# Performance work log

Hardware: AMD Instinct MI355X
Metric: run time of the kernel (lower is better)

The kernel has to match this reference:

```python
import jax, jax.numpy as jnp
import numpy as np

NUM_HEADS = 16
EPS = 1e-12  # matches torch F.normalize eps


def _l2_normalize(x):
    n = jnp.sqrt(jnp.sum(x * x, axis=-1, keepdims=True))
    return x / jnp.maximum(n, EPS)


def setup_inputs() -> dict:
    key = jax.random.key(0)
    ks = jax.random.split(key, 9)
    B, L, S, D = 4, 4096, 4096, 1024
    s = 1.0 / np.sqrt(D)
    return {
        "q": jax.random.normal(ks[0], (B, L, D), jnp.float32),
        "k": jax.random.normal(ks[1], (B, S, D), jnp.float32),
        "v": jax.random.normal(ks[2], (B, S, D), jnp.float32),
        "Wq": jax.random.normal(ks[3], (D, D), jnp.float32) * s,
        "bq": jax.random.normal(ks[4], (D,), jnp.float32) * 0.01,
        "Wk": jax.random.normal(ks[5], (D, D), jnp.float32) * s,
        "bk": jax.random.normal(ks[6], (D,), jnp.float32) * 0.01,
        "Wv": jax.random.normal(ks[7], (D, D), jnp.float32) * s,
        "bv": jax.random.normal(ks[8], (D,), jnp.float32) * 0.01,
    }


def reference(q, k, v, Wq, bq, Wk, bk, Wv, bv):
    B = q.shape[0]
    H = NUM_HEADS
    # Linear projections (torch Linear: x @ W^T + b)
    qp = q @ Wq.T + bq  # [B, L, D]
    kp = k @ Wk.T + bk  # [B, S, D]
    vp = v @ Wv.T + bv  # [B, S, D]
    # Split heads: [B, T, H, i] -> [B, H, T, i]
    def split(x):
        Bx, T, D = x.shape
        return x.reshape(Bx, T, H, D // H).transpose(0, 2, 1, 3)
    qh = split(qp)
    kh = _l2_normalize(split(kp))
    vh = _l2_normalize(split(vp))
    # No softmax -> exact reassociation: (q k^T) v == q (k^T v)
    kv = jnp.einsum('bhsi,bhsj->bhij', kh, vh)  # [B, H, i, i]
    xh = jnp.einsum('bhli,bhij->bhlj', qh, kv)  # [B, H, L, i]
    # Merge heads: [B, H, L, i] -> [B, L, H*i]
    Bx, Hh, L, I = xh.shape
    return xh.transpose(0, 2, 1, 3).reshape(Bx, L, Hh * I)
```

## Files before the change

### kernel.cpp

```cpp
#include <hip/hip_runtime.h>
#include <hip/hip_bf16.h>
#include <stdint.h>

typedef __attribute__((ext_vector_type(8))) short bf16x8;
typedef __attribute__((ext_vector_type(4))) float f32x4;
typedef __attribute__((ext_vector_type(8))) unsigned short ushort8;

__device__ __forceinline__ float bf2f(unsigned short u) {
  union { unsigned int i; float f; } x; x.i = ((unsigned int)u) << 16; return x.f;
}
__device__ __forceinline__ unsigned short f2bf(float f) {
  union { __hip_bfloat16 h; unsigned short u; } x; x.h = __float2bfloat16(f); return x.u;
}

__device__ __forceinline__ void gload_lds16(const void* g, void* l) {
  __builtin_amdgcn_global_load_lds((__attribute__((address_space(1))) const void*)g,
                                   (__attribute__((address_space(3))) void*)l, 16, 0, 0);
}

__global__ __launch_bounds__(256) void cvt_kernel(const float* __restrict__ in,
                                                  unsigned short* __restrict__ out,
                                                  int n8) {
  int i = blockIdx.x * 256 + threadIdx.x;
  if (i >= n8) return;
  const float4* p = (const float4*)(in + (size_t)i * 8);
  float4 a = p[0], b = p[1];
  ushort8 o;
  o[0] = f2bf(a.x); o[1] = f2bf(a.y); o[2] = f2bf(a.z); o[3] = f2bf(a.w);
  o[4] = f2bf(b.x); o[5] = f2bf(b.y); o[6] = f2bf(b.z); o[7] = f2bf(b.w);
  *(ushort8*)(out + (size_t)i * 8) = o;
}

__global__ __launch_bounds__(256) void cvt2_kernel(const float* __restrict__ a,
                                                   const float* __restrict__ b,
                                                   unsigned short* __restrict__ oa,
                                                   unsigned short* __restrict__ ob,
                                                   int n8) {
  const float* in = blockIdx.y ? b : a;
  unsigned short* out = blockIdx.y ? ob : oa;
  int i = blockIdx.x * 256 + threadIdx.x;
  if (i >= n8) return;
  const float4* p = (const float4*)(in + (size_t)i * 8);
  float4 x = p[0], y = p[1];
  ushort8 o;
  o[0] = f2bf(x.x); o[1] = f2bf(x.y); o[2] = f2bf(x.z); o[3] = f2bf(x.w);
  o[4] = f2bf(y.x); o[5] = f2bf(y.y); o[6] = f2bf(y.z); o[7] = f2bf(y.w);
  *(ushort8*)(out + (size_t)i * 8) = o;
}

__global__ __launch_bounds__(256) void cvt3w_kernel(const float* __restrict__ a,
                                                    const float* __restrict__ b,
                                                    const float* __restrict__ c,
                                                    unsigned short* __restrict__ oa,
                                                    unsigned short* __restrict__ ob,
                                                    unsigned short* __restrict__ oc,
                                                    int n8) {
  const float* in = blockIdx.y == 0 ? a : blockIdx.y == 1 ? b : c;
  unsigned short* out = blockIdx.y == 0 ? oa : blockIdx.y == 1 ? ob : oc;
  int i = blockIdx.x * 256 + threadIdx.x;
  if (i >= n8) return;
  const float4* p = (const float4*)(in + (size_t)i * 8);
  float4 x = p[0], y = p[1];
  ushort8 o;
  o[0] = f2bf(x.x); o[1] = f2bf(x.y); o[2] = f2bf(x.z); o[3] = f2bf(x.w);
  o[4] = f2bf(y.x); o[5] = f2bf(y.y); o[6] = f2bf(y.z); o[7] = f2bf(y.w);
  *(ushort8*)(out + (size_t)i * 8) = o;
}

__device__ __forceinline__ void gemm256_loop(
    const unsigned short* __restrict__ A,
    const unsigned short* __restrict__ B,
    int bm, int bn,
    unsigned short (*As)[256][32], unsigned short (*Bs)[256][32],
    f32x4 (*acc)[4]) {
  const int tid = threadIdx.x;
  const int widx = tid >> 6, lane = tid & 63;
  const int wr = widx >> 2, wc = widx & 3;
  const int fr = lane & 15, fkg = lane >> 4;
  const int pgo = (fkg ^ ((fr >> 1) & 3)) * 8;
  const int srow = lane >> 2;
  const int sg = ((lane & 3) ^ ((lane >> 3) & 3)) * 8;

  const size_t abase = (size_t)(bm * 256) * 1024;
  const size_t bbase = (size_t)(bn * 256) * 1024;

  bf16x8 aF[8], bF[4];

#define STG_A(bufi, kh, kt)                                                                \
  {                                                                                        \
    gload_lds16(A + abase + (size_t)(widx * 16 + srow) * 1024 + (kt) * 64 + (kh) * 32 + sg,\
                &As[(bufi) * 2 + (kh)][widx * 16][0]);                                     \
    gload_lds16(A + abase + (size_t)(128 + widx * 16 + srow) * 1024 + (kt) * 64 + (kh) * 32 + sg, \
                &As[(bufi) * 2 + (kh)][128 + widx * 16][0]);                               \
  }
#define STG_B(bufi, kh, kt)                                                                \
  {                                                                                        \
    gload_lds16(B + bbase + (size_t)(widx * 16 + srow) * 1024 + (kt) * 64 + (kh) * 32 + sg,\
                &Bs[(bufi) * 2 + (kh)][widx * 16][0]);                                     \
    gload_lds16(B + bbase + (size_t)(128 + widx * 16 + srow) * 1024 + (kt) * 64 + (kh) * 32 + sg, \
                &Bs[(bufi) * 2 + (kh)][128 + widx * 16][0]);                               \
  }
#define LDA(bufi, ks)                                                                      \
  _Pragma("unroll") for (int m = 0; m < 8; ++m)                                            \
      aF[m] = *(const bf16x8*)&As[(bufi) * 2 + (ks)][wr * 128 + m * 16 + fr][pgo];
#define LDBALL(bufi, ks)                                                                   \
  _Pragma("unroll") for (int n = 0; n < 4; ++n)                                            \
      bF[n] = *(const bf16x8*)&Bs[(bufi) * 2 + (ks)][wc * 64 + n * 16 + fr][pgo];
#define MMALL()                                                                            \
  {                                                                                        \
    __builtin_amdgcn_s_setprio(1);                                                         \
    _Pragma("unroll") for (int m = 0; m < 8; ++m)                                          \
        _Pragma("unroll") for (int n = 0; n < 4; ++n)                                      \
            acc[m][n] = __builtin_amdgcn_mfma_f32_16x16x32_bf16(aF[m], bF[n], acc[m][n], 0, 0, 0); \
    __builtin_amdgcn_s_setprio(0);                                                         \
  }
#define BARM() asm volatile("s_barrier" ::: "memory")
#define VMW(N) asm volatile("s_waitcnt vmcnt(" #N ")" ::: "memory")

  STG_A(0, 0, 0); STG_B(0, 0, 0);
  STG_A(0, 1, 0); STG_B(0, 1, 0);
  STG_A(1, 0, 1); STG_B(1, 0, 1);
  VMW(4);
  BARM();

  for (int i = 0; i < 8; ++i) {
    const int t1s = 2 * i + 1, u0 = 2 * i + 2, u1 = 2 * i + 3;
    const bool st = (i < 7);
    LDA(0, 0); LDBALL(0, 0); STG_A(1, 1, t1s); STG_B(1, 1, t1s);
    BARM(); MMALL(); BARM();
    LDA(0, 1); LDBALL(0, 1); if (st) { STG_A(0, 0, u0); STG_B(0, 0, u0); }
    BARM(); MMALL();
    if (st) { VMW(4); } else { VMW(0); }
    BARM();
    LDA(1, 0); LDBALL(1, 0); if (st) { STG_A(0, 1, u0); STG_B(0, 1, u0); }
    BARM(); MMALL(); BARM();
    LDA(1, 1); LDBALL(1, 1); if (st) { STG_A(1, 0, u1); STG_B(1, 0, u1); }
    BARM(); MMALL();
    if (st) { VMW(4); } else { VMW(0); }
    BARM();
  }
#undef STG_A
#undef STG_B
#undef LDA
#undef LDBALL
#undef MMALL
#undef BARM
#undef VMW
}

__global__ __launch_bounds__(512, 1) void proj_norm_kernel(
    const unsigned short* __restrict__ A0, const unsigned short* __restrict__ A1,
    const unsigned short* __restrict__ B0, const unsigned short* __restrict__ B1,
    const float* __restrict__ bias0, const float* __restrict__ bias1,
    unsigned short* __restrict__ C0, unsigned short* __restrict__ C1) {
  __shared__ unsigned short As[4][256][32];
  __shared__ unsigned short Bs[4][256][32];
  const int flat = (blockIdx.z * 64 + blockIdx.y) * 4 + blockIdx.x;
  const int swz = (flat & 7) * 64 + (flat >> 3);
  const int zz = swz >> 8;
  const int rem = swz & 255;
  const int bm = rem >> 2, bn = rem & 3;
  const unsigned short* A = zz ? A1 : A0;
  const unsigned short* B = zz ? B1 : B0;
  const float* bias = zz ? bias1 : bias0;
  unsigned short* C = zz ? C1 : C0;

  f32x4 acc[8][4];
#pragma unroll
  for (int m = 0; m < 8; ++m)
#pragma unroll
    for (int n = 0; n < 4; ++n) acc[m][n] = (f32x4){0.f, 0.f, 0.f, 0.f};

  gemm256_loop(A, B, bm, bn, As, Bs, acc);

  const int tid = threadIdx.x, widx = tid >> 6, lane = tid & 63;
  const int wr = widx >> 2, wc = widx & 3;
  const int fr = lane & 15, g4 = (lane >> 4) * 4;

  float bsv[4];
#pragma unroll
  for (int n = 0; n < 4; ++n) bsv[n] = bias[bn * 256 + wc * 64 + n * 16 + fr];
#pragma unroll
  for (int m = 0; m < 8; ++m) {
    float val[4][4];
    float inv[4];
#pragma unroll
    for (int j = 0; j < 4; ++j) {
      float s = 0.f;
#pragma unroll
      for (int n = 0; n < 4; ++n) {
        val[n][j] = acc[m][n][j] + bsv[n];
        s += val[n][j] * val[n][j];
      }
      s += __shfl_xor(s, 1); s += __shfl_xor(s, 2);
      s += __shfl_xor(s, 4); s += __shfl_xor(s, 8);
      inv[j] = 1.f / fmaxf(sqrtf(s), 1e-12f);
    }
#pragma unroll
    for (int n = 0; n < 4; ++n) {
      const int col = bn * 256 + wc * 64 + n * 16 + fr;
#pragma unroll
      for (int j = 0; j < 4; ++j) {
        const int row = bm * 256 + wr * 128 + m * 16 + g4 + j;
        C[(size_t)row * 1024 + col] = f2bf(val[n][j] * inv[j]);
      }
    }
  }
}

__global__ __launch_bounds__(512, 1) void final_fold_kernel(
    const unsigned short* __restrict__ A,
    const unsigned short* __restrict__ Wqb,
    const float* __restrict__ bq,
    const unsigned short* __restrict__ kvT,
    float* __restrict__ out) {
  __shared__ __align__(16) unsigned char smem[163840];
  unsigned short (*As)[256][32] = (unsigned short (*)[256][32])smem;
  unsigned short (*Bs)[256][32] = (unsigned short (*)[256][32])(smem + 65536);

  const int flat = blockIdx.y * 4 + blockIdx.x;
  const int swz = (flat & 7) * 32 + (flat >> 3);
  const int bm = swz >> 2, bn = swz & 3;
  const int bB = bm >> 4;

  const int tid = threadIdx.x, widx = tid >> 6, lane = tid & 63;
  const int wr = widx >> 2, wc = widx & 3;
  const int fr = lane & 15, fkg = lane >> 4, g4 = fkg * 4;

#pragma unroll
  for (int t = 0; t < 4; ++t) {
    int unit = t * 512 + tid;
    int h = unit >> 9;
    int jr = (unit >> 3) & 63;
    int g = unit & 7;
    ushort8 vvv = *(const ushort8*)(kvT +
        ((size_t)(bB * 16 + bn * 4 + h) * 4096) + jr * 64 + g * 8);
    *(ushort8*)(smem + 131072 + h * 8192 + jr * 128 + ((g ^ (jr & 7)) * 16)) = vvv;
  }
  __syncthreads();

  f32x4 acc[8][4];
#pragma unroll
  for (int m = 0; m < 8; ++m)
#pragma unroll
    for (int n = 0; n < 4; ++n) acc[m][n] = (f32x4){0.f, 0.f, 0.f, 0.f};

  gemm256_loop(A, Wqb, bm, bn, As, Bs, acc);

  {
    float bsv[4];
#pragma unroll
    for (int n = 0; n < 4; ++n) bsv[n] = bq[bn * 256 + wc * 64 + n * 16 + fr];
#pragma unroll
    for (int m = 0; m < 8; ++m)
#pragma unroll
      for (int n = 0; n < 4; ++n)
#pragma unroll
        for (int j = 0; j < 4; ++j) {
          float v = acc[m][n][j] + bsv[n];
          int r = m * 16 + g4 + j;
          int c = n * 16 + fr;
          *(unsigned short*)(smem + widx * 16384 + r * 128 +
                             (((c >> 3) ^ (r & 7)) * 16) + (c & 7) * 2) = f2bf(v);
        }
  }
  __syncthreads();

  f32x4 acc2[8][4];
#pragma unroll
  for (int m = 0; m < 8; ++m)
#pragma unroll
    for (int n = 0; n < 4; ++n) acc2[m][n] = (f32x4){0.f, 0.f, 0.f, 0.f};

#pragma unroll
  for (int ks = 0; ks < 2; ++ks) {
    bf16x8 a2[8], b2[4];
#pragma unroll
    for (int m = 0; m < 8; ++m)
      a2[m] = *(const bf16x8*)(smem + widx * 16384 + (m * 16 + fr) * 128 +
                               (((ks * 4 + fkg) ^ (fr & 7)) * 16));
#pragma unroll
    for (int n = 0; n < 4; ++n)
      b2[n] = *(const bf16x8*)(smem + 131072 + wc * 8192 + (n * 16 + fr) * 128 +
                               (((ks * 4 + fkg) ^ (fr & 7)) * 16));
#pragma unroll
    for (int m = 0; m < 8; ++m)
#pragma unroll
      for (int n = 0; n < 4; ++n)
        acc2[m][n] = __builtin_amdgcn_mfma_f32_16x16x32_bf16(a2[m], b2[n], acc2[m][n], 0, 0, 0);
  }

#pragma unroll
  for (int n = 0; n < 4; ++n) {
    const int col = bn * 256 + wc * 64 + n * 16 + fr;
#pragma unroll
    for (int m = 0; m < 8; ++m)
#pragma unroll
      for (int j = 0; j < 4; ++j) {
        const int row = bm * 256 + wr * 128 + m * 16 + g4 + j;
        out[(size_t)row * 1024 + col] = acc2[m][n][j];
      }
  }
}

__global__ __launch_bounds__(256) void kv_part_kernel(const unsigned short* __restrict__ kh,
                                                      const unsigned short* __restrict__ vh,
                                                      float* __restrict__ kvp) {
  const int chunk = blockIdx.x, h = blockIdx.y, b = blockIdx.z;
  __shared__ unsigned short khT[64][264];
  __shared__ unsigned short vhT[64][264];
  const int tid = threadIdx.x, wid = tid >> 6, lane = tid & 63;
  const int fr = lane & 15, fk = (lane >> 4) * 8, g4 = (lane >> 4) * 4;

  const int jb = tid & 7, sb = tid >> 3;
  const size_t base = ((size_t)b * 4096 + chunk * 256) * 1024 + h * 64;
  {
    ushort8 rk[8], rv[8];
#pragma unroll
    for (int u = 0; u < 8; ++u) {
      rk[u] = *(const ushort8*)(kh + base + (size_t)(sb * 8 + u) * 1024 + jb * 8);
      rv[u] = *(const ushort8*)(vh + base + (size_t)(sb * 8 + u) * 1024 + jb * 8);
    }
#pragma unroll
    for (int jj = 0; jj < 8; ++jj) {
      ushort8 ck, cv;
#pragma unroll
      for (int u = 0; u < 8; ++u) { ck[u] = rk[u][jj]; cv[u] = rv[u][jj]; }
      *(ushort8*)&khT[jb * 8 + jj][sb * 8] = ck;
      *(ushort8*)&vhT[jb * 8 + jj][sb * 8] = cv;
    }
  }
  __syncthreads();

  f32x4 acc2[4];
#pragma unroll
  for (int n = 0; n < 4; ++n) acc2[n] = (f32x4){0.f, 0.f, 0.f, 0.f};
#pragma unroll
  for (int ks = 0; ks < 8; ++ks) {
    bf16x8 a2 = *(const bf16x8*)&khT[wid * 16 + fr][ks * 32 + fk];
    bf16x8 b2[4];
#pragma unroll
    for (int jt = 0; jt < 4; ++jt) b2[jt] = *(const bf16x8*)&vhT[jt * 16 + fr][ks * 32 + fk];
#pragma unroll
    for (int jt = 0; jt < 4; ++jt)
      acc2[jt] = __builtin_amdgcn_mfma_f32_16x16x32_bf16(a2, b2[jt], acc2[jt], 0, 0, 0);
  }
  float* dst = kvp + ((size_t)chunk * 64 + b * 16 + h) * 4096;
#pragma unroll
  for (int jt = 0; jt < 4; ++jt)
#pragma unroll
    for (int jj = 0; jj < 4; ++jj)
      dst[(wid * 16 + g4 + jj) * 64 + jt * 16 + fr] = acc2[jt][jj];
}

__global__ __launch_bounds__(256) void kvt_reduce_kernel(const float* __restrict__ kvp,
                                                         unsigned short* __restrict__ kvT) {
  const int bh = blockIdx.x;
  for (int e = threadIdx.x; e < 4096; e += 256) {
    float s = 0.f;
#pragma unroll
    for (int c = 0; c < 16; ++c) s += kvp[((size_t)c * 64 + bh) * 4096 + e];
    int i = e >> 6, j = e & 63;
    kvT[(size_t)bh * 4096 + j * 64 + i] = f2bf(s);
  }
}

extern "C" void kernel_launch(void* const* d_in, const int* in_sizes, int n_in,
                              void* d_out, int out_size, void* d_ws, size_t ws_size,
                              hipStream_t stream) {
  const float* q = (const float*)d_in[0];
  const float* k = (const float*)d_in[1];
  const float* v = (const float*)d_in[2];
  const float* Wq = (const float*)d_in[3];
  const float* bq = (const float*)d_in[4];
  const float* Wk = (const float*)d_in[5];
  const float* bk = (const float*)d_in[6];
  const float* Wv = (const float*)d_in[7];
  const float* bv = (const float*)d_in[8];
  float* out = (float*)d_out;

  const size_t NE = (size_t)16384 * 1024;
  const size_t MB = 1048576;

  char* ws = (char*)d_ws;
  unsigned short* S0 = (unsigned short*)(ws + 0 * MB);
  unsigned short* S1 = (unsigned short*)(ws + 32 * MB);
  unsigned short* kh = (unsigned short*)(ws + 64 * MB);
  unsigned short* vh = (unsigned short*)(ws + 96 * MB);
  unsigned short* Wqb = (unsigned short*)(ws + 128 * MB);
  unsigned short* Wkb = (unsigned short*)(ws + 130 * MB);
  unsigned short* Wvb = (unsigned short*)(ws + 132 * MB);
  unsigned short* kvT = (unsigned short*)(ws + 134 * MB);
  float* kvp = (float*)S0;

  cvt2_kernel<<<dim3(8192, 2), 256, 0, stream>>>(k, v, S0, S1, (int)(NE / 8));
  cvt3w_kernel<<<dim3(512, 3), 256, 0, stream>>>(Wq, Wk, Wv, Wqb, Wkb, Wvb, 131072);

  proj_norm_kernel<<<dim3(4, 64, 2), 512, 0, stream>>>(S0, S1, Wkb, Wvb, bk, bv, kh, vh);

  cvt_kernel<<<8192, 256, 0, stream>>>(q, S1, (int)(NE / 8));

  kv_part_kernel<<<dim3(16, 16, 4), 256, 0, stream>>>(kh, vh, kvp);

  kvt_reduce_kernel<<<64, 256, 0, stream>>>(kvp, kvT);

  final_fold_kernel<<<dim3(4, 64), 512, 0, stream>>>(S1, Wqb, bq, kvT, out);
}
```

Baseline: 213.6 us.

## Fuse K/V projection, normalization and per-chunk KV partial product into one kernel

The K and V projections are now computed by the same block, back to back, over the same 256-row by 256-column tile. The L2-normalized bf16 results stay in registers and are staged through swizzled LDS, where the block computes the partial k^T v product for its four heads directly. This removes the global write and reread of the normalized kh/vh tensors and drops the separate kv_part launch. The q conversion is also merged into a single three-input convert launch. In exchange, each block now runs two GEMMs serially with a grid half the size, 256 blocks instead of 512, and needs more registers to hold the packed kh/vh values.

Result: slower. 300.5 us (+40.7%).

```diff
diff --git a/kernel.cpp b/kernel.cpp
--- a/kernel.cpp
+++ b/kernel.cpp
@@ -18,43 +18,13 @@
                                    (__attribute__((address_space(3))) void*)l, 16, 0, 0);
 }
 
-__global__ __launch_bounds__(256) void cvt_kernel(const float* __restrict__ in,
-                                                  unsigned short* __restrict__ out,
-                                                  int n8) {
-  int i = blockIdx.x * 256 + threadIdx.x;
-  if (i >= n8) return;
-  const float4* p = (const float4*)(in + (size_t)i * 8);
-  float4 a = p[0], b = p[1];
-  ushort8 o;
-  o[0] = f2bf(a.x); o[1] = f2bf(a.y); o[2] = f2bf(a.z); o[3] = f2bf(a.w);
-  o[4] = f2bf(b.x); o[5] = f2bf(b.y); o[6] = f2bf(b.z); o[7] = f2bf(b.w);
-  *(ushort8*)(out + (size_t)i * 8) = o;
-}
-
-__global__ __launch_bounds__(256) void cvt2_kernel(const float* __restrict__ a,
+__global__ __launch_bounds__(256) void cvt3_kernel(const float* __restrict__ a,
                                                    const float* __restrict__ b,
+                                                   const float* __restrict__ c,
                                                    unsigned short* __restrict__ oa,
                                                    unsigned short* __restrict__ ob,
+                                                   unsigned short* __restrict__ oc,
                                                    int n8) {
-  const float* in = blockIdx.y ? b : a;
-  unsigned short* out = blockIdx.y ? ob : oa;
-  int i = blockIdx.x * 256 + threadIdx.x;
-  if (i >= n8) return;
-  const float4* p = (const float4*)(in + (size_t)i * 8);
-  float4 x = p[0], y = p[1];
-  ushort8 o;
-  o[0] = f2bf(x.x); o[1] = f2bf(x.y); o[2] = f2bf(x.z); o[3] = f2bf(x.w);
-  o[4] = f2bf(y.x); o[5] = f2bf(y.y); o[6] = f2bf(y.z); o[7] = f2bf(y.w);
-  *(ushort8*)(out + (size_t)i * 8) = o;
-}
-
-__global__ __launch_bounds__(256) void cvt3w_kernel(const float* __restrict__ a,
-                                                    const float* __restrict__ b,
-                                                    const float* __restrict__ c,
-                                                    unsigned short* __restrict__ oa,
-                                                    unsigned short* __restrict__ ob,
-                                                    unsigned short* __restrict__ oc,
-                                                    int n8) {
   const float* in = blockIdx.y == 0 ? a : blockIdx.y == 1 ? b : c;
   unsigned short* out = blockIdx.y == 0 ? oa : blockIdx.y == 1 ? ob : oc;
   int i = blockIdx.x * 256 + threadIdx.x;
@@ -148,64 +118,144 @@
 #undef VMW
 }
 
-__global__ __launch_bounds__(512, 1) void proj_norm_kernel(
-    const unsigned short* __restrict__ A0, const unsigned short* __restrict__ A1,
-    const unsigned short* __restrict__ B0, const unsigned short* __restrict__ B1,
-    const float* __restrict__ bias0, const float* __restrict__ bias1,
-    unsigned short* __restrict__ C0, unsigned short* __restrict__ C1) {
+__global__ __launch_bounds__(512, 1) void projkv_kernel(
+    const unsigned short* __restrict__ kbf,
+    const unsigned short* __restrict__ vbf,
+    const unsigned short* __restrict__ Wkb,
+    const unsigned short* __restrict__ Wvb,
+    const float* __restrict__ bkb,
+    const float* __restrict__ bvb,
+    float* __restrict__ kvp) {
   __shared__ unsigned short As[4][256][32];
   __shared__ unsigned short Bs[4][256][32];
-  const int flat = (blockIdx.z * 64 + blockIdx.y) * 4 + blockIdx.x;
-  const int swz = (flat & 7) * 64 + (flat >> 3);
-  const int zz = swz >> 8;
-  const int rem = swz & 255;
-  const int bm = rem >> 2, bn = rem & 3;
-  const unsigned short* A = zz ? A1 : A0;
-  const unsigned short* B = zz ? B1 : B0;
-  const float* bias = zz ? bias1 : bias0;
-  unsigned short* C = zz ? C1 : C0;
-
-  f32x4 acc[8][4];
-#pragma unroll
-  for (int m = 0; m < 8; ++m)
-#pragma unroll
-    for (int n = 0; n < 4; ++n) acc[m][n] = (f32x4){0.f, 0.f, 0.f, 0.f};
-
-  gemm256_loop(A, B, bm, bn, As, Bs, acc);
+  const int flat = blockIdx.y * 4 + blockIdx.x;
+  const int swz = (flat & 7) * 32 + (flat >> 3);
+  const int bm = swz >> 2, bn = swz & 3;
 
   const int tid = threadIdx.x, widx = tid >> 6, lane = tid & 63;
   const int wr = widx >> 2, wc = widx & 3;
-  const int fr = lane & 15, g4 = (lane >> 4) * 4;
-
-  float bsv[4];
-#pragma unroll
-  for (int n = 0; n < 4; ++n) bsv[n] = bias[bn * 256 + wc * 64 + n * 16 + fr];
-#pragma unroll
-  for (int m = 0; m < 8; ++m) {
-    float val[4][4];
-    float inv[4];
-#pragma unroll
-    for (int j = 0; j < 4; ++j) {
-      float s = 0.f;
-#pragma unroll
-      for (int n = 0; n < 4; ++n) {
-        val[n][j] = acc[m][n][j] + bsv[n];
-        s += val[n][j] * val[n][j];
+  const int fr = lane & 15, fkg = lane >> 4, g4 = fkg * 4;
+
+  f32x4 acc[8][4];
+  unsigned short khp[8][4][4], vhp[8][4][4];
+
+#pragma unroll
+  for (int m = 0; m < 8; ++m)
+#pragma unroll
+    for (int n = 0; n < 4; ++n) acc[m][n] = (f32x4){0.f, 0.f, 0.f, 0.f};
+  gemm256_loop(kbf, Wkb, bm, bn, As, Bs, acc);
+  {
+    float bsv[4];
+#pragma unroll
+    for (int n = 0; n < 4; ++n) bsv[n] = bkb[bn * 256 + wc * 64 + n * 16 + fr];
+#pragma unroll
+    for (int m = 0; m < 8; ++m) {
+      float val[4][4], inv[4];
+#pragma unroll
+      for (int j = 0; j < 4; ++j) {
+        float s = 0.f;
+#pragma unroll
+        for (int n = 0; n < 4; ++n) {
+          val[n][j] = acc[m][n][j] + bsv[n];
+          s += val[n][j] * val[n][j];
+        }
+        s += __shfl_xor(s, 1); s += __shfl_xor(s, 2);
+        s += __shfl_xor(s, 4); s += __shfl_xor(s, 8);
+        inv[j] = 1.f / fmaxf(sqrtf(s), 1e-12f);
       }
-      s += __shfl_xor(s, 1); s += __shfl_xor(s, 2);
-      s += __shfl_xor(s, 4); s += __shfl_xor(s, 8);
-      inv[j] = 1.f / fmaxf(sqrtf(s), 1e-12f);
+#pragma unroll
+      for (int n = 0; n < 4; ++n)
+#pragma unroll
+        for (int j = 0; j < 4; ++j) khp[m][n][j] = f2bf(val[n][j] * inv[j]);
     }
-#pragma unroll
-    for (int n = 0; n < 4; ++n) {
-      const int col = bn * 256 + wc * 64 + n * 16 + fr;
+  }
+
+#pragma unroll
+  for (int m = 0; m < 8; ++m)
+#pragma unroll
+    for (int n = 0; n < 4; ++n) acc[m][n] = (f32x4){0.f, 0.f, 0.f, 0.f};
+  gemm256_loop(vbf, Wvb, bm, bn, As, Bs, acc);
+  {
+    float bsv[4];
+#pragma unroll
+    for (int n = 0; n < 4; ++n) bsv[n] = bvb[bn * 256 + wc * 64 + n * 16 + fr];
+#pragma unroll
+    for (int m = 0; m < 8; ++m) {
+      float val[4][4], inv[4];
 #pragma unroll
       for (int j = 0; j < 4; ++j) {
-        const int row = bm * 256 + wr * 128 + m * 16 + g4 + j;
-        C[(size_t)row * 1024 + col] = f2bf(val[n][j] * inv[j]);
+        float s = 0.f;
+#pragma unroll
+        for (int n = 0; n < 4; ++n) {
+          val[n][j] = acc[m][n][j] + bsv[n];
+          s += val[n][j] * val[n][j];
+        }
+        s += __shfl_xor(s, 1); s += __shfl_xor(s, 2);
+        s += __shfl_xor(s, 4); s += __shfl_xor(s, 8);
+        inv[j] = 1.f / fmaxf(sqrtf(s), 1e-12f);
       }
+#pragma unroll
+      for (int n = 0; n < 4; ++n)
+#pragma unroll
+        for (int j = 0; j < 4; ++j) vhp[m][n][j] = f2bf(val[n][j] * inv[j]);
     }
   }
+
+  unsigned char* khT = (unsigned char*)&As[0][0][0];
+  unsigned char* vhT = (unsigned char*)&Bs[0][0][0];
+  f32x4 acc2[2][4];
+#pragma unroll
+  for (int mi = 0; mi < 2; ++mi)
+#pragma unroll
+    for (int nj = 0; nj < 4; ++nj) acc2[mi][nj] = (f32x4){0.f, 0.f, 0.f, 0.f};
+
+#pragma unroll
+  for (int p = 0; p < 2; ++p) {
+    __syncthreads();
+    if (wr == p) {
+#pragma unroll
+      for (int m = 0; m < 8; ++m)
+#pragma unroll
+        for (int n = 0; n < 4; ++n)
+#pragma unroll
+          for (int j = 0; j < 4; ++j) {
+            const int s = m * 16 + g4 + j;
+            const int i = n * 16 + fr;
+            const int off = wc * 16384 + i * 256 + (((s >> 3) ^ (i & 7)) * 16) + (s & 7) * 2;
+            *(unsigned short*)(khT + off) = khp[m][n][j];
+            *(unsigned short*)(vhT + off) = vhp[m][n][j];
+          }
+    }
+    __syncthreads();
+#pragma unroll
+    for (int ks = 0; ks < 4; ++ks) {
+      bf16x8 a2[2], b2[4];
+#pragma unroll
+      for (int mi = 0; mi < 2; ++mi) {
+        const int i = wr * 32 + mi * 16 + fr;
+        a2[mi] = *(const bf16x8*)(khT + wc * 16384 + i * 256 + (((ks * 4 + fkg) ^ (i & 7)) * 16));
+      }
+#pragma unroll
+      for (int nj = 0; nj < 4; ++nj) {
+        const int j = nj * 16 + fr;
+        b2[nj] = *(const bf16x8*)(vhT + wc * 16384 + j * 256 + (((ks * 4 + fkg) ^ (j & 7)) * 16));
+      }
+#pragma unroll
+      for (int mi = 0; mi < 2; ++mi)
+#pragma unroll
+        for (int nj = 0; nj < 4; ++nj)
+          acc2[mi][nj] = __builtin_amdgcn_mfma_f32_16x16x32_bf16(a2[mi], b2[nj], acc2[mi][nj], 0, 0, 0);
+    }
+  }
+
+  float* dst = kvp + ((size_t)(bm & 15) * 64 + (size_t)(bm >> 4) * 16 + bn * 4 + wc) * 4096;
+#pragma unroll
+  for (int mi = 0; mi < 2; ++mi)
+#pragma unroll
+    for (int nj = 0; nj < 4; ++nj)
+#pragma unroll
+      for (int jj = 0; jj < 4; ++jj)
+        dst[(wr * 32 + mi * 16 + g4 + jj) * 64 + nj * 16 + fr] = acc2[mi][nj][jj];
 }
 
 __global__ __launch_bounds__(512, 1) void final_fold_kernel(
@@ -301,56 +351,6 @@
         out[(size_t)row * 1024 + col] = acc2[m][n][j];
       }
   }
-}
-
-__global__ __launch_bounds__(256) void kv_part_kernel(const unsigned short* __restrict__ kh,
-                                                      const unsigned short* __restrict__ vh,
-                                                      float* __restrict__ kvp) {
-  const int chunk = blockIdx.x, h = blockIdx.y, b = blockIdx.z;
-  __shared__ unsigned short khT[64][264];
-  __shared__ unsigned short vhT[64][264];
-  const int tid = threadIdx.x, wid = tid >> 6, lane = tid & 63;
-  const int fr = lane & 15, fk = (lane >> 4) * 8, g4 = (lane >> 4) * 4;
-
-  const int jb = tid & 7, sb = tid >> 3;
-  const size_t base = ((size_t)b * 4096 + chunk * 256) * 1024 + h * 64;
-  {
-    ushort8 rk[8], rv[8];
-#pragma unroll
-    for (int u = 0; u < 8; ++u) {
-      rk[u] = *(const ushort8*)(kh + base + (size_t)(sb * 8 + u) * 1024 + jb * 8);
-      rv[u] = *(const ushort8*)(vh + base + (size_t)(sb * 8 + u) * 1024 + jb * 8);
-    }
-#pragma unroll
-    for (int jj = 0; jj < 8; ++jj) {
-      ushort8 ck, cv;
-#pragma unroll
-      for (int u = 0; u < 8; ++u) { ck[u] = rk[u][jj]; cv[u] = rv[u][jj]; }
-      *(ushort8*)&khT[jb * 8 + jj][sb * 8] = ck;
-      *(ushort8*)&vhT[jb * 8 + jj][sb * 8] = cv;
-    }
-  }
-  __syncthreads();
-
-  f32x4 acc2[4];
-#pragma unroll
-  for (int n = 0; n < 4; ++n) acc2[n] = (f32x4){0.f, 0.f, 0.f, 0.f};
-#pragma unroll
-  for (int ks = 0; ks < 8; ++ks) {
-    bf16x8 a2 = *(const bf16x8*)&khT[wid * 16 + fr][ks * 32 + fk];
-    bf16x8 b2[4];
-#pragma unroll
-    for (int jt = 0; jt < 4; ++jt) b2[jt] = *(const bf16x8*)&vhT[jt * 16 + fr][ks * 32 + fk];
-#pragma unroll
-    for (int jt = 0; jt < 4; ++jt)
-      acc2[jt] = __builtin_amdgcn_mfma_f32_16x16x32_bf16(a2, b2[jt], acc2[jt], 0, 0, 0);
-  }
-  float* dst = kvp + ((size_t)chunk * 64 + b * 16 + h) * 4096;
-#pragma unroll
-  for (int jt = 0; jt < 4; ++jt)
-#pragma unroll
-    for (int jj = 0; jj < 4; ++jj)
-      dst[(wid * 16 + g4 + jj) * 64 + jt * 16 + fr] = acc2[jt][jj];
 }
 
 __global__ __launch_bounds__(256) void kvt_reduce_kernel(const float* __restrict__ kvp,
@@ -383,26 +383,21 @@
   const size_t MB = 1048576;
 
   char* ws = (char*)d_ws;
-  unsigned short* S0 = (unsigned short*)(ws + 0 * MB);
-  unsigned short* S1 = (unsigned short*)(ws + 32 * MB);
-  unsigned short* kh = (unsigned short*)(ws + 64 * MB);
-  unsigned short* vh = (unsigned short*)(ws + 96 * MB);
-  unsigned short* Wqb = (unsigned short*)(ws + 128 * MB);
-  unsigned short* Wkb = (unsigned short*)(ws + 130 * MB);
-  unsigned short* Wvb = (unsigned short*)(ws + 132 * MB);
-  unsigned short* kvT = (unsigned short*)(ws + 134 * MB);
-  float* kvp = (float*)S0;
-
-  cvt2_kernel<<<dim3(8192, 2), 256, 0, stream>>>(k, v, S0, S1, (int)(NE / 8));
-  cvt3w_kernel<<<dim3(512, 3), 256, 0, stream>>>(Wq, Wk, Wv, Wqb, Wkb, Wvb, 131072);
-
-  proj_norm_kernel<<<dim3(4, 64, 2), 512, 0, stream>>>(S0, S1, Wkb, Wvb, bk, bv, kh, vh);
-
-  cvt_kernel<<<8192, 256, 0, stream>>>(q, S1, (int)(NE / 8));
-
-  kv_part_kernel<<<dim3(16, 16, 4), 256, 0, stream>>>(kh, vh, kvp);
+  unsigned short* kbf = (unsigned short*)(ws + 0 * MB);
+  unsigned short* vbf = (unsigned short*)(ws + 32 * MB);
+  unsigned short* qbf = (unsigned short*)(ws + 64 * MB);
+  float* kvp = (float*)(ws + 96 * MB);
+  unsigned short* Wqb = (unsigned short*)(ws + 112 * MB);
+  unsigned short* Wkb = (unsigned short*)(ws + 114 * MB);
+  unsigned short* Wvb = (unsigned short*)(ws + 116 * MB);
+  unsigned short* kvT = (unsigned short*)(ws + 118 * MB);
+
+  cvt3_kernel<<<dim3(8192, 3), 256, 0, stream>>>(q, k, v, qbf, kbf, vbf, (int)(NE / 8));
+  cvt3_kernel<<<dim3(512, 3), 256, 0, stream>>>(Wq, Wk, Wv, Wqb, Wkb, Wvb, 131072);
+
+  projkv_kernel<<<dim3(4, 64), 512, 0, stream>>>(kbf, vbf, Wkb, Wvb, bk, bv, kvp);
 
   kvt_reduce_kernel<<<64, 256, 0, stream>>>(kvp, kvT);
 
-  final_fold_kernel<<<dim3(4, 64), 512, 0, stream>>>(S1, Wqb, bq, kvT, out);
-}
+  final_fold_kernel<<<dim3(4, 64), 512, 0, stream>>>(qbf, Wqb, bq, kvT, out);
+}
```
